# Kernel optimization log

Measured on AMD Instinct MI355X. Metric: run time of the kernel, lower is better.

## Reference

```python
import jax, jax.numpy as jnp
import numpy as np

ANCHORS = jnp.array([[0.57273, 0.677385], [1.87446, 2.06253], [3.33843, 5.47434],
                     [7.88282, 3.52778], [9.77052, 9.16828]], dtype=jnp.float32)
IOU_THR = 0.6
SCALE_NOOBJ = 1.0
SCALE_OBJ = 5.0
DS = 32.0          # downsample_rate
EPS = 1e-7


def _iou_wh(w1, h1, w2, h2):
    # GetCenterAlignIouBetween: boxes aligned at centers -> IoU depends on w,h only
    inter = jnp.minimum(w1, w2) * jnp.minimum(h1, h2)
    return inter / (w1 * h1 + w2 * h2 - inter + EPS)


def setup_inputs() -> dict:
    B, W, H, A, C, M = 128, 19, 19, 5, 81, 24
    N = W * H
    key = jax.random.key(0)
    ks = jax.random.split(key, 8)
    ii, jj = jnp.meshgrid(jnp.arange(W), jnp.arange(H), indexing='ij')
    fm_cord = jnp.stack([jj, ii], -1).reshape(N, 2).astype(jnp.float32)  # (x=j, y=i)
    conf = jax.random.uniform(ks[0], (B, W, H, A, 1)) * 0.98 + 0.01      # valid BCE probs
    pred_xy = fm_cord.reshape(1, W, H, 1, 2) + jax.random.uniform(ks[1], (B, W, H, A, 2))
    pred_wh = jax.random.uniform(ks[2], (B, W, H, A, 2)) * 8.0 + 0.2     # fm units, >0
    cls_score = jax.random.normal(ks[3], (B, W, H, A, C))
    # distinct grid cells per image so sequential scatter == vectorized scatter
    cells = jax.vmap(lambda k: jax.random.choice(k, N, (M,), replace=False))(
        jax.random.split(ks[4], B))
    ci = cells // H
    cj = cells % H
    frac = jax.random.uniform(ks[5], (B, M, 2))
    x = (cj.astype(jnp.float32) + frac[..., 0]) * DS   # pixel coords
    y = (ci.astype(jnp.float32) + frac[..., 1]) * DS
    wh = jax.random.uniform(ks[6], (B, M, 2), minval=12.0, maxval=280.0)
    true_object = jnp.stack([x, y, wh[..., 0], wh[..., 1]], -1)          # [B,M,4] pixels
    labels = jax.random.randint(ks[7], (B, M), 0, C - 1)
    true_label = jax.nn.one_hot(labels, C, dtype=jnp.float32)            # [B,M,C]
    return dict(epoch=0, conf=conf, pred_xy=pred_xy, pred_wh=pred_wh,
                cls_score=cls_score, true_label=true_label,
                true_object=true_object, fm_cord=fm_cord)


def _yolo_loss(conf, pred_xy, pred_wh, cls_score, true_label, true_object, fm_cord):
    B, W, H, A, C = cls_score.shape
    N = W * H
    NA = N * A
    S = float(W)  # config.output_size

    # ---- target assignment (vectorized version of the python loops) ----
    obj = true_object / DS                               # fm units, [B,M,4]
    gx, gy, gw, gh = obj[..., 0], obj[..., 1], obj[..., 2], obj[..., 3]
    i = gy.astype(jnp.int32)                             # row index  (int() truncation)
    j = gx.astype(jnp.int32)                             # col index
    cell = i * H + j                                     # flat cell, [B,M]

    a_iou = _iou_wh(ANCHORS[None, None, :, 0], ANCHORS[None, None, :, 1],
                    gw[..., None], gh[..., None])        # [B,M,A]
    best = jnp.argmax(a_iou, axis=-1)                    # [B,M]
    is_best = best[..., None] == jnp.arange(A)[None, None, :]
    over = a_iou > IOU_THR

    bb = jnp.arange(B)[:, None]
    pwh = pred_wh.reshape(B, N, A, 2)[bb, cell]          # [B,M,A,2] gather at gt cells
    pwh_b = jnp.take_along_axis(pwh, best[..., None, None], axis=2)[:, :, 0]  # [B,M,2]
    iou_pg = _iou_wh(pwh_b[..., 0], pwh_b[..., 1], gw, gh)                    # [B,M]

    mask_val = jnp.where(is_best, 1.0, jnp.where(over, -1.0, 0.0))            # [B,M,A]
    sw = 2.0 - (gw / S) * (gh / S)                                            # [B,M]
    sw_val = jnp.where(is_best, sw[..., None], jnp.where(over, -1.0, 0.0))
    pgi_val = jnp.where(~is_best & over, 0.0, iou_pg[..., None])              # [B,M,A]
    bg = jax.nn.one_hot(C - 1, C, dtype=cls_score.dtype)
    ts_val = jnp.where((is_best | over)[..., None], true_label[:, :, None, :], bg)
    bbox_val = jnp.where(is_best[..., None], obj[:, :, None, :], 0.0)         # [B,M,A,4]

    obj_mask = jnp.zeros((B, N, A)).at[bb, cell].set(mask_val)
    scale_w = jnp.zeros((B, N, A)).at[bb, cell].set(sw_val)
    pgi = jnp.zeros((B, N, A)).at[bb, cell].set(pgi_val)
    true_score = jnp.zeros((B, N, A, C)).at[..., -1].set(1.0).at[bb, cell].set(ts_val)
    true_bbox = jnp.zeros((B, N, A, 4)).at[bb, cell].set(bbox_val)

    # ---- masked losses over flattened [B, W*H*A, ...] ----
    conf_f = conf.reshape(B, NA)
    om = obj_mask.reshape(B, NA)
    swf = scale_w.reshape(B, NA)
    pgif = pgi.reshape(B, NA)
    pxy = pred_xy.reshape(B, NA, 2)
    pwh_f = pred_wh.reshape(B, NA, 2)
    tb = true_bbox.reshape(B, NA, 4)
    ts = true_score.reshape(B, NA, C)
    cs = cls_score.reshape(B, NA, C)
    cord = jnp.repeat(fm_cord[:, None, :], A, axis=1).reshape(NA, 2)

    cp = jnp.clip(conf_f, EPS, 1.0 - EPS)
    noobj_loss = SCALE_NOOBJ * jnp.sum((om == 0) * (-jnp.log(1.0 - cp))) / B
    obj_loss = SCALE_OBJ * jnp.sum(
        (om == 1) * (-(pgif * jnp.log(cp) + (1.0 - pgif) * jnp.log(1.0 - cp)))) / B

    gt = (swf > 0).astype(conf_f.dtype)                  # [B,NA]
    w3 = (SCALE_OBJ * gt * swf)[..., None]
    xy_loss = jnp.sum(w3 * ((pxy - cord[None]) - (tb[..., :2] - cord[None])) ** 2) / B
    wh_loss = jnp.sum(w3 * (pwh_f - tb[..., 2:]) ** 2) / B

    # CE with soft targets, per position: [B,NA]
    ce = -jnp.sum(ts * jax.nn.log_softmax(cs, axis=-1), axis=-1)
    # original broadcasts mask [B,1,NA] * ce [B,NA] -> [B,B,NA] then .sum();
    # equivalent factored form: sum_n (sum_b1 mask) * (sum_b2 ce)
    score_loss = SCALE_OBJ * jnp.sum(gt.sum(0) * ce.sum(0)) / B

    total = noobj_loss + obj_loss + xy_loss + wh_loss + score_loss
    return total, noobj_loss, obj_loss, score_loss, xy_loss, wh_loss


def reference(epoch, conf, pred_xy, pred_wh, cls_score, true_label, true_object, fm_cord):
    return _yolo_loss(conf, pred_xy, pred_wh, cls_score,
                      true_label, true_object, fm_cord)
```

## Files before the change

### kernel.cpp

```cpp
#include <hip/hip_runtime.h>

#define Bsz 128
#define Cd 81
#define Md 24
#define Nd 361
#define NAd 1805
#define RPW 16
#define NT 113
#define NBLK_CLS (NT*16)
#define NOBJ (Bsz*Md)
#define NBLK_LAB (NOBJ/RPW)
#define EPSF 1e-7f
#define IOU_THRF 0.6f

#define OFF_CORR  0
#define OFF_GT    1824
#define OFF_ACC   3648
#define MEMSET_FLOATS 3652
#define OFF_PART  4096
#define OFF_NOOBJ 33024
#define OFF_LAB   35072

#define EXP4(v) { v.x=__expf(v.x); v.y=__expf(v.y); v.z=__expf(v.z); v.w=__expf(v.w); }

__global__ __launch_bounds__(64) void yolo_sweep(
        const float* __restrict__ conf,
        const float* __restrict__ cls_score,
        const float* __restrict__ true_label,
        float* __restrict__ ws) {
    __shared__ float ex[1300];
    const int lane = threadIdx.x;
    const int r = lane >> 2, h = lane & 3;
    const int bid = blockIdx.x;
    float4* l4 = (float4*)ex;

    if (bid < NBLK_CLS) {
        const int t = bid >> 4, g = bid & 15;
        const int na0 = (t == NT - 1) ? (NAd - RPW) : t * RPW;
        const int vmin = t * RPW;
        const bool validr = (na0 + r) >= vmin;
        const bool validc = (lane < RPW) && ((na0 + lane) >= vmin);

        float accCE = 0.0f, nb = 0.0f;

        size_t s = ((size_t)(g * 8) * NAd + na0) * Cd;
        size_t a0 = s & ~(size_t)3;
        int mcur = (int)(s & 3);
        const float4* gp = (const float4*)cls_score + (a0 >> 2);
        float4 u0 = gp[0 * 64 + lane];
        float4 u1 = gp[1 * 64 + lane];
        float4 u2 = gp[2 * 64 + lane];
        float4 u3 = gp[3 * 64 + lane];
        float4 u4 = gp[4 * 64 + lane];
        float4 u5 = gp[261 + lane];
        float cf = validc ? conf[(size_t)(g * 8) * NAd + na0 + lane] : 0.5f;

        for (int it = 0; it < 8; ++it) {
            EXP4(u0); EXP4(u1); EXP4(u2); EXP4(u3); EXP4(u4); EXP4(u5);
            l4[0 * 64 + lane] = u0;
            l4[1 * 64 + lane] = u1;
            l4[2 * 64 + lane] = u2;
            l4[3 * 64 + lane] = u3;
            l4[4 * 64 + lane] = u4;
            l4[261 + lane] = u5;
            __builtin_amdgcn_wave_barrier();

            float4 n0 = {}, n1 = {}, n2 = {}, n3 = {}, n4 = {}, n5 = {};
            float cfn = 0.0f; int mnext = 0;
            if (it < 7) {
                int b = g * 8 + it + 1;
                s = ((size_t)b * NAd + na0) * Cd;
                a0 = s & ~(size_t)3;
                mnext = (int)(s & 3);
                gp = (const float4*)cls_score + (a0 >> 2);
                n0 = gp[0 * 64 + lane];
                n1 = gp[1 * 64 + lane];
                n2 = gp[2 * 64 + lane];
                n3 = gp[3 * 64 + lane];
                n4 = gp[4 * 64 + lane];
                n5 = gp[261 + lane];
                cfn = validc ? conf[(size_t)b * NAd + na0 + lane] : 0.5f;
            }

            const float* p = ex + mcur + r * Cd;
            float sacc = 0.0f;
            #pragma unroll
            for (int j = 0; j < 21; j++) {
                int c0 = h * 21 + j;
                int cc = c0 < 81 ? c0 : 80;
                float w = (c0 < 81) ? 1.0f : 0.0f;
                sacc += p[cc] * w;
            }
            sacc += __shfl_xor(sacc, 1, 64);
            sacc += __shfl_xor(sacc, 2, 64);
            if (h == 0 && validr)
                accCE += __logf(sacc) - __logf(p[80]);
            if (validc) {
                float cp = fminf(fmaxf(cf, EPSF), 1.0f - EPSF);
                nb += -__logf(1.0f - cp);
            }

            u0 = n0; u1 = n1; u2 = n2; u3 = n3; u4 = n4; u5 = n5;
            cf = cfn; mcur = mnext;
        }

        if (h == 0 && validr)
            ws[OFF_PART + (size_t)(na0 + r) * 16 + g] = accCE;

        #pragma unroll
        for (int off = 32; off > 0; off >>= 1) nb += __shfl_xor(nb, off, 64);
        if (lane == 0) ws[OFF_NOOBJ + bid] = nb;
    } else {
        const int lb = bid - NBLK_CLS;
        const float4* gp = (const float4*)(true_label + (size_t)lb * (RPW * Cd));
        float4 u0 = gp[0 * 64 + lane];
        float4 u1 = gp[1 * 64 + lane];
        float4 u2 = gp[2 * 64 + lane];
        float4 u3 = gp[3 * 64 + lane];
        float4 u4 = gp[4 * 64 + lane];
        float4 u5 = gp[260 + lane];
        l4[0 * 64 + lane] = u0;
        l4[1 * 64 + lane] = u1;
        l4[2 * 64 + lane] = u2;
        l4[3 * 64 + lane] = u3;
        l4[4 * 64 + lane] = u4;
        l4[260 + lane] = u5;
        __builtin_amdgcn_wave_barrier();
        const float* p = ex + r * Cd;
        float sacc = 0.0f;
        #pragma unroll
        for (int j = 0; j < 21; j++) {
            int c0 = h * 21 + j;
            int cc = c0 < 81 ? c0 : 80;
            float w = (c0 < 81) ? (float)c0 : 0.0f;
            sacc += p[cc] * w;
        }
        sacc += __shfl_xor(sacc, 1, 64);
        sacc += __shfl_xor(sacc, 2, 64);
        if (h == 0) ws[OFF_LAB + lb * RPW + r] = sacc;
    }
}

__global__ __launch_bounds__(64) void yolo_assign(
        const float* __restrict__ conf,
        const float* __restrict__ pred_xy,
        const float* __restrict__ pred_wh,
        const float* __restrict__ cls_score,
        const float* __restrict__ true_object,
        float* __restrict__ ws) {
    const float AW[5] = {0.57273f, 1.87446f, 3.33843f, 7.88282f, 9.77052f};
    const float AH[5] = {0.677385f, 2.06253f, 5.47434f, 3.52778f, 9.16828f};
    const int idx = blockIdx.x * 64 + threadIdx.x;
    float* corr = ws + OFF_CORR;
    float* gt   = ws + OFF_GT;

    int lab = (int)(ws[OFF_LAB + idx] + 0.5f);
    int b = idx / Md;
    const float4 to = ((const float4*)true_object)[idx];
    const float inv_ds = 1.0f / 32.0f;
    float gx = to.x * inv_ds, gy = to.y * inv_ds;
    float gw = to.z * inv_ds, gh = to.w * inv_ds;
    int ci = (int)gy, cj = (int)gx;
    int cell = ci * 19 + cj;
    float garea = gw * gh;

    float best_iou = -1.0f; int best = 0; bool over[5];
    #pragma unroll
    for (int a = 0; a < 5; a++) {
        float inter = fminf(AW[a], gw) * fminf(AH[a], gh);
        float iou = inter / (AW[a] * AH[a] + garea - inter + EPSF);
        over[a] = iou > IOU_THRF;
        if (iou > best_iou) { best_iou = iou; best = a; }
    }

    int base_bn = (b * Nd + cell) * 5;
    float pwb = pred_wh[(size_t)(base_bn + best) * 2 + 0];
    float phb = pred_wh[(size_t)(base_bn + best) * 2 + 1];
    float inter = fminf(pwb, gw) * fminf(phb, gh);
    float iou_pg = inter / (pwb * phb + garea - inter + EPSF);
    float sw = 2.0f - (gw * (1.0f / 19.0f)) * (gh * (1.0f / 19.0f));

    float a0 = 0.f, a1 = 0.f, a2 = 0.f, a3 = 0.f;
    #pragma unroll
    for (int a = 0; a < 5; a++) {
        bool isb = (a == best);
        if (!(isb || over[a])) continue;
        int pos = base_bn + a;
        int na  = cell * 5 + a;
        float cp = fminf(fmaxf(conf[pos], EPSF), 1.0f - EPSF);
        a0 += __logf(1.0f - cp);
        const float* cs = cls_score + (size_t)pos * Cd;
        atomicAdd(&corr[na], cs[Cd - 1] - cs[lab]);
        if (isb) {
            atomicAdd(&gt[na], 1.0f);
            a1 += -(iou_pg * __logf(cp) + (1.0f - iou_pg) * __logf(1.0f - cp));
            float px = pred_xy[(size_t)pos * 2 + 0], py = pred_xy[(size_t)pos * 2 + 1];
            a2 += sw * ((px - gx) * (px - gx) + (py - gy) * (py - gy));
            float pwa = pred_wh[(size_t)pos * 2 + 0], pha = pred_wh[(size_t)pos * 2 + 1];
            a3 += sw * ((pwa - gw) * (pwa - gw) + (pha - gh) * (pha - gh));
        }
    }

    #pragma unroll
    for (int off = 32; off > 0; off >>= 1) {
        a0 += __shfl_xor(a0, off, 64);
        a1 += __shfl_xor(a1, off, 64);
        a2 += __shfl_xor(a2, off, 64);
        a3 += __shfl_xor(a3, off, 64);
    }
    if (threadIdx.x == 0) {
        atomicAdd(&ws[OFF_ACC + 0], a0);
        atomicAdd(&ws[OFF_ACC + 1], a1);
        atomicAdd(&ws[OFF_ACC + 2], a2);
        atomicAdd(&ws[OFF_ACC + 3], a3);
    }
}

__global__ __launch_bounds__(1024) void yolo_reduce(
        const float* __restrict__ ws, float* __restrict__ out) {
    __shared__ float red[2][16];
    const int tid = threadIdx.x;
    float nsum = 0.0f;
    for (int i = tid; i < NBLK_CLS; i += 1024) nsum += ws[OFF_NOOBJ + i];
    float ssum = 0.0f;
    const float4* part4 = (const float4*)(ws + OFF_PART);
    for (int na = tid; na < NAd; na += 1024) {
        float4 p0 = part4[na * 4 + 0];
        float4 p1 = part4[na * 4 + 1];
        float4 p2 = part4[na * 4 + 2];
        float4 p3 = part4[na * 4 + 3];
        float ce = p0.x + p0.y + p0.z + p0.w + p1.x + p1.y + p1.z + p1.w
                 + p2.x + p2.y + p2.z + p2.w + p3.x + p3.y + p3.z + p3.w
                 + ws[OFF_CORR + na];
        ssum += ws[OFF_GT + na] * ce;
    }

    float v[2] = {nsum, ssum};
    #pragma unroll
    for (int k = 0; k < 2; k++) {
        float x = v[k];
        #pragma unroll
        for (int off = 32; off > 0; off >>= 1) x += __shfl_xor(x, off, 64);
        if ((tid & 63) == 0) red[k][tid >> 6] = x;
    }
    __syncthreads();
    if (tid == 0) {
        float t0 = 0.f, t1 = 0.f;
        #pragma unroll
        for (int w = 0; w < 16; w++) { t0 += red[0][w]; t1 += red[1][w]; }
        const float invB = 1.0f / (float)Bsz;
        float noobj = 1.0f * (t0 + ws[OFF_ACC + 0]) * invB;
        float obj   = 5.0f * ws[OFF_ACC + 1] * invB;
        float xy    = 5.0f * ws[OFF_ACC + 2] * invB;
        float wh    = 5.0f * ws[OFF_ACC + 3] * invB;
        float score = 5.0f * t1 * invB;
        out[0] = noobj + obj + xy + wh + score;
        out[1] = noobj;
        out[2] = obj;
        out[3] = score;
        out[4] = xy;
        out[5] = wh;
    }
}

extern "C" void kernel_launch(void* const* d_in, const int* in_sizes, int n_in,
                              void* d_out, int out_size, void* d_ws, size_t ws_size,
                              hipStream_t stream) {
    const float* conf    = (const float*)d_in[1];
    const float* pred_xy = (const float*)d_in[2];
    const float* pred_wh = (const float*)d_in[3];
    const float* cls     = (const float*)d_in[4];
    const float* tlabel  = (const float*)d_in[5];
    const float* tobject = (const float*)d_in[6];
    float* ws  = (float*)d_ws;
    float* out = (float*)d_out;

    hipMemsetAsync(ws, 0, MEMSET_FLOATS * sizeof(float), stream);

    yolo_sweep<<<NBLK_CLS + NBLK_LAB, 64, 0, stream>>>(conf, cls, tlabel, ws);

    yolo_assign<<<NOBJ / 64, 64, 0, stream>>>(conf, pred_xy, pred_wh, cls, tobject, ws);

    yolo_reduce<<<1, 1024, 0, stream>>>(ws, out);
}
```

Measured before the change: 130.8 us.

## Fuse sweep, assign and reduce into one kernel with last-block reduction

Merges the three kernels into one launch. Assignment blocks compute the label index directly from one-hot rows instead of through a separate pass. The final reduction is done by the last block to arrive at an atomic counter. This removes launch overhead and inter-kernel gaps, but the final reduce now runs on a single 64-thread wave, and label reads are per-thread strided.

Result: slower. 204.4 us (+56.2%).

```diff
diff --git a/kernel.cpp b/kernel.cpp
--- a/kernel.cpp
+++ b/kernel.cpp
@@ -7,35 +7,112 @@
 #define NAd 1805
 #define RPW 16
 #define NT 113
+#define NBLK_ASSIGN 48
 #define NBLK_CLS (NT*16)
+#define NBLK_TOT (NBLK_ASSIGN + NBLK_CLS)
 #define NOBJ (Bsz*Md)
-#define NBLK_LAB (NOBJ/RPW)
 #define EPSF 1e-7f
 #define IOU_THRF 0.6f
 
 #define OFF_CORR  0
 #define OFF_GT    1824
 #define OFF_ACC   3648
-#define MEMSET_FLOATS 3652
+#define OFF_CNT   3652
+#define MEMSET_FLOATS 3656
 #define OFF_PART  4096
 #define OFF_NOOBJ 33024
-#define OFF_LAB   35072
 
 #define EXP4(v) { v.x=__expf(v.x); v.y=__expf(v.y); v.z=__expf(v.z); v.w=__expf(v.w); }
 
-__global__ __launch_bounds__(64) void yolo_sweep(
+__global__ __launch_bounds__(64) void yolo_mega(
         const float* __restrict__ conf,
+        const float* __restrict__ pred_xy,
+        const float* __restrict__ pred_wh,
         const float* __restrict__ cls_score,
         const float* __restrict__ true_label,
-        float* __restrict__ ws) {
+        const float* __restrict__ true_object,
+        float* __restrict__ ws,
+        float* __restrict__ out) {
     __shared__ float ex[1300];
     const int lane = threadIdx.x;
-    const int r = lane >> 2, h = lane & 3;
     const int bid = blockIdx.x;
-    float4* l4 = (float4*)ex;
-
-    if (bid < NBLK_CLS) {
-        const int t = bid >> 4, g = bid & 15;
+
+    if (bid < NBLK_ASSIGN) {
+        const float AW[5] = {0.57273f, 1.87446f, 3.33843f, 7.88282f, 9.77052f};
+        const float AH[5] = {0.677385f, 2.06253f, 5.47434f, 3.52778f, 9.16828f};
+        const int idx = bid * 64 + lane;
+        float* corr = ws + OFF_CORR;
+        float* gt   = ws + OFF_GT;
+
+        const float* tl = true_label + (size_t)idx * Cd;
+        float labf = 0.0f;
+        #pragma unroll
+        for (int c0 = 0; c0 < Cd; c0++) labf += tl[c0] * (float)c0;
+        int lab = (int)(labf + 0.5f);
+
+        int b = idx / Md;
+        const float4 to = ((const float4*)true_object)[idx];
+        const float inv_ds = 1.0f / 32.0f;
+        float gx = to.x * inv_ds, gy = to.y * inv_ds;
+        float gw = to.z * inv_ds, gh = to.w * inv_ds;
+        int ci = (int)gy, cj = (int)gx;
+        int cell = ci * 19 + cj;
+        float garea = gw * gh;
+
+        float best_iou = -1.0f; int best = 0; bool over[5];
+        #pragma unroll
+        for (int a = 0; a < 5; a++) {
+            float inter = fminf(AW[a], gw) * fminf(AH[a], gh);
+            float iou = inter / (AW[a] * AH[a] + garea - inter + EPSF);
+            over[a] = iou > IOU_THRF;
+            if (iou > best_iou) { best_iou = iou; best = a; }
+        }
+
+        int base_bn = (b * Nd + cell) * 5;
+        float pwb = pred_wh[(size_t)(base_bn + best) * 2 + 0];
+        float phb = pred_wh[(size_t)(base_bn + best) * 2 + 1];
+        float inter = fminf(pwb, gw) * fminf(phb, gh);
+        float iou_pg = inter / (pwb * phb + garea - inter + EPSF);
+        float sw = 2.0f - (gw * (1.0f / 19.0f)) * (gh * (1.0f / 19.0f));
+
+        float a0 = 0.f, a1 = 0.f, a2 = 0.f, a3 = 0.f;
+        #pragma unroll
+        for (int a = 0; a < 5; a++) {
+            bool isb = (a == best);
+            if (!(isb || over[a])) continue;
+            int pos = base_bn + a;
+            int na  = cell * 5 + a;
+            float cp = fminf(fmaxf(conf[pos], EPSF), 1.0f - EPSF);
+            a0 += __logf(1.0f - cp);
+            const float* cs = cls_score + (size_t)pos * Cd;
+            atomicAdd(&corr[na], cs[Cd - 1] - cs[lab]);
+            if (isb) {
+                atomicAdd(&gt[na], 1.0f);
+                a1 += -(iou_pg * __logf(cp) + (1.0f - iou_pg) * __logf(1.0f - cp));
+                float px = pred_xy[(size_t)pos * 2 + 0], py = pred_xy[(size_t)pos * 2 + 1];
+                a2 += sw * ((px - gx) * (px - gx) + (py - gy) * (py - gy));
+                float pwa = pred_wh[(size_t)pos * 2 + 0], pha = pred_wh[(size_t)pos * 2 + 1];
+                a3 += sw * ((pwa - gw) * (pwa - gw) + (pha - gh) * (pha - gh));
+            }
+        }
+        #pragma unroll
+        for (int off = 32; off > 0; off >>= 1) {
+            a0 += __shfl_xor(a0, off, 64);
+            a1 += __shfl_xor(a1, off, 64);
+            a2 += __shfl_xor(a2, off, 64);
+            a3 += __shfl_xor(a3, off, 64);
+        }
+        if (lane == 0) {
+            atomicAdd(&ws[OFF_ACC + 0], a0);
+            atomicAdd(&ws[OFF_ACC + 1], a1);
+            atomicAdd(&ws[OFF_ACC + 2], a2);
+            atomicAdd(&ws[OFF_ACC + 3], a3);
+        }
+    } else {
+        const int cbid = bid - NBLK_ASSIGN;
+        const int r = lane >> 2, h = lane & 3;
+        float4* l4 = (float4*)ex;
+        const int t = cbid >> 4, g = cbid & 15;
         const int na0 = (t == NT - 1) ? (NAd - RPW) : t * RPW;
         const int vmin = t * RPW;
         const bool validr = (na0 + r) >= vmin;
@@ -44,9 +121,9 @@
         float accCE = 0.0f, nb = 0.0f;
 
         size_t s = ((size_t)(g * 8) * NAd + na0) * Cd;
-        size_t a0 = s & ~(size_t)3;
+        size_t a0a = s & ~(size_t)3;
         int mcur = (int)(s & 3);
-        const float4* gp = (const float4*)cls_score + (a0 >> 2);
+        const float4* gp = (const float4*)cls_score + (a0a >> 2);
         float4 u0 = gp[0 * 64 + lane];
         float4 u1 = gp[1 * 64 + lane];
         float4 u2 = gp[2 * 64 + lane];
@@ -70,9 +147,9 @@
             if (it < 7) {
                 int b = g * 8 + it + 1;
                 s = ((size_t)b * NAd + na0) * Cd;
-                a0 = s & ~(size_t)3;
+                a0a = s & ~(size_t)3;
                 mnext = (int)(s & 3);
-                gp = (const float4*)cls_score + (a0 >> 2);
+                gp = (const float4*)cls_score + (a0a >> 2);
                 n0 = gp[0 * 64 + lane];
                 n1 = gp[1 * 64 + lane];
                 n2 = gp[2 * 64 + lane];
@@ -88,8 +165,7 @@
             for (int j = 0; j < 21; j++) {
                 int c0 = h * 21 + j;
                 int cc = c0 < 81 ? c0 : 80;
-                float w = (c0 < 81) ? 1.0f : 0.0f;
-                sacc += p[cc] * w;
+                sacc += p[cc] * ((c0 < 81) ? 1.0f : 0.0f);
             }
             sacc += __shfl_xor(sacc, 1, 64);
             sacc += __shfl_xor(sacc, 2, 64);
@@ -106,160 +182,50 @@
 
         if (h == 0 && validr)
             ws[OFF_PART + (size_t)(na0 + r) * 16 + g] = accCE;
-
         #pragma unroll
         for (int off = 32; off > 0; off >>= 1) nb += __shfl_xor(nb, off, 64);
-        if (lane == 0) ws[OFF_NOOBJ + bid] = nb;
-    } else {
-        const int lb = bid - NBLK_CLS;
-        const float4* gp = (const float4*)(true_label + (size_t)lb * (RPW * Cd));
-        float4 u0 = gp[0 * 64 + lane];
-        float4 u1 = gp[1 * 64 + lane];
-        float4 u2 = gp[2 * 64 + lane];
-        float4 u3 = gp[3 * 64 + lane];
-        float4 u4 = gp[4 * 64 + lane];
-        float4 u5 = gp[260 + lane];
-        l4[0 * 64 + lane] = u0;
-        l4[1 * 64 + lane] = u1;
-        l4[2 * 64 + lane] = u2;
-        l4[3 * 64 + lane] = u3;
-        l4[4 * 64 + lane] = u4;
-        l4[260 + lane] = u5;
-        __builtin_amdgcn_wave_barrier();
-        const float* p = ex + r * Cd;
-        float sacc = 0.0f;
-        #pragma unroll
-        for (int j = 0; j < 21; j++) {
-            int c0 = h * 21 + j;
-            int cc = c0 < 81 ? c0 : 80;
-            float w = (c0 < 81) ? (float)c0 : 0.0f;
-            sacc += p[cc] * w;
-        }
-        sacc += __shfl_xor(sacc, 1, 64);
-        sacc += __shfl_xor(sacc, 2, 64);
-        if (h == 0) ws[OFF_LAB + lb * RPW + r] = sacc;
+        if (lane == 0) ws[OFF_NOOBJ + cbid] = nb;
     }
-}
-
-__global__ __launch_bounds__(64) void yolo_assign(
-        const float* __restrict__ conf,
-        const float* __restrict__ pred_xy,
-        const float* __restrict__ pred_wh,
-        const float* __restrict__ cls_score,
-        const float* __restrict__ true_object,
-        float* __restrict__ ws) {
-    const float AW[5] = {0.57273f, 1.87446f, 3.33843f, 7.88282f, 9.77052f};
-    const float AH[5] = {0.677385f, 2.06253f, 5.47434f, 3.52778f, 9.16828f};
-    const int idx = blockIdx.x * 64 + threadIdx.x;
-    float* corr = ws + OFF_CORR;
-    float* gt   = ws + OFF_GT;
-
-    int lab = (int)(ws[OFF_LAB + idx] + 0.5f);
-    int b = idx / Md;
-    const float4 to = ((const float4*)true_object)[idx];
-    const float inv_ds = 1.0f / 32.0f;
-    float gx = to.x * inv_ds, gy = to.y * inv_ds;
-    float gw = to.z * inv_ds, gh = to.w * inv_ds;
-    int ci = (int)gy, cj = (int)gx;
-    int cell = ci * 19 + cj;
-    float garea = gw * gh;
-
-    float best_iou = -1.0f; int best = 0; bool over[5];
-    #pragma unroll
-    for (int a = 0; a < 5; a++) {
-        float inter = fminf(AW[a], gw) * fminf(AH[a], gh);
-        float iou = inter / (AW[a] * AH[a] + garea - inter + EPSF);
-        over[a] = iou > IOU_THRF;
-        if (iou > best_iou) { best_iou = iou; best = a; }
-    }
-
-    int base_bn = (b * Nd + cell) * 5;
-    float pwb = pred_wh[(size_t)(base_bn + best) * 2 + 0];
-    float phb = pred_wh[(size_t)(base_bn + best) * 2 + 1];
-    float inter = fminf(pwb, gw) * fminf(phb, gh);
-    float iou_pg = inter / (pwb * phb + garea - inter + EPSF);
-    float sw = 2.0f - (gw * (1.0f / 19.0f)) * (gh * (1.0f / 19.0f));
-
-    float a0 = 0.f, a1 = 0.f, a2 = 0.f, a3 = 0.f;
-    #pragma unroll
-    for (int a = 0; a < 5; a++) {
-        bool isb = (a == best);
-        if (!(isb || over[a])) continue;
-        int pos = base_bn + a;
-        int na  = cell * 5 + a;
-        float cp = fminf(fmaxf(conf[pos], EPSF), 1.0f - EPSF);
-        a0 += __logf(1.0f - cp);
-        const float* cs = cls_score + (size_t)pos * Cd;
-        atomicAdd(&corr[na], cs[Cd - 1] - cs[lab]);
-        if (isb) {
-            atomicAdd(&gt[na], 1.0f);
-            a1 += -(iou_pg * __logf(cp) + (1.0f - iou_pg) * __logf(1.0f - cp));
-            float px = pred_xy[(size_t)pos * 2 + 0], py = pred_xy[(size_t)pos * 2 + 1];
-            a2 += sw * ((px - gx) * (px - gx) + (py - gy) * (py - gy));
-            float pwa = pred_wh[(size_t)pos * 2 + 0], pha = pred_wh[(size_t)pos * 2 + 1];
-            a3 += sw * ((pwa - gw) * (pwa - gw) + (pha - gh) * (pha - gh));
-        }
-    }
-
-    #pragma unroll
-    for (int off = 32; off > 0; off >>= 1) {
-        a0 += __shfl_xor(a0, off, 64);
-        a1 += __shfl_xor(a1, off, 64);
-        a2 += __shfl_xor(a2, off, 64);
-        a3 += __shfl_xor(a3, off, 64);
-    }
-    if (threadIdx.x == 0) {
-        atomicAdd(&ws[OFF_ACC + 0], a0);
-        atomicAdd(&ws[OFF_ACC + 1], a1);
-        atomicAdd(&ws[OFF_ACC + 2], a2);
-        atomicAdd(&ws[OFF_ACC + 3], a3);
-    }
-}
-
-__global__ __launch_bounds__(1024) void yolo_reduce(
-        const float* __restrict__ ws, float* __restrict__ out) {
-    __shared__ float red[2][16];
-    const int tid = threadIdx.x;
-    float nsum = 0.0f;
-    for (int i = tid; i < NBLK_CLS; i += 1024) nsum += ws[OFF_NOOBJ + i];
-    float ssum = 0.0f;
-    const float4* part4 = (const float4*)(ws + OFF_PART);
-    for (int na = tid; na < NAd; na += 1024) {
-        float4 p0 = part4[na * 4 + 0];
-        float4 p1 = part4[na * 4 + 1];
-        float4 p2 = part4[na * 4 + 2];
-        float4 p3 = part4[na * 4 + 3];
-        float ce = p0.x + p0.y + p0.z + p0.w + p1.x + p1.y + p1.z + p1.w
-                 + p2.x + p2.y + p2.z + p2.w + p3.x + p3.y + p3.z + p3.w
-                 + ws[OFF_CORR + na];
-        ssum += ws[OFF_GT + na] * ce;
-    }
-
-    float v[2] = {nsum, ssum};
-    #pragma unroll
-    for (int k = 0; k < 2; k++) {
-        float x = v[k];
-        #pragma unroll
-        for (int off = 32; off > 0; off >>= 1) x += __shfl_xor(x, off, 64);
-        if ((tid & 63) == 0) red[k][tid >> 6] = x;
-    }
-    __syncthreads();
-    if (tid == 0) {
-        float t0 = 0.f, t1 = 0.f;
-        #pragma unroll
-        for (int w = 0; w < 16; w++) { t0 += red[0][w]; t1 += red[1][w]; }
-        const float invB = 1.0f / (float)Bsz;
-        float noobj = 1.0f * (t0 + ws[OFF_ACC + 0]) * invB;
-        float obj   = 5.0f * ws[OFF_ACC + 1] * invB;
-        float xy    = 5.0f * ws[OFF_ACC + 2] * invB;
-        float wh    = 5.0f * ws[OFF_ACC + 3] * invB;
-        float score = 5.0f * t1 * invB;
-        out[0] = noobj + obj + xy + wh + score;
-        out[1] = noobj;
-        out[2] = obj;
-        out[3] = score;
-        out[4] = xy;
-        out[5] = wh;
+
+    __threadfence();
+    unsigned old = 0;
+    if (lane == 0) old = atomicAdd((unsigned*)(ws + OFF_CNT), 1u);
+    old = __shfl(old, 0, 64);
+    if (old == NBLK_TOT - 1) {
+        __threadfence();
+        float nsum = 0.0f;
+        for (int i = lane; i < NBLK_CLS; i += 64) nsum += ws[OFF_NOOBJ + i];
+        float ssum = 0.0f;
+        const float4* part4 = (const float4*)(ws + OFF_PART);
+        for (int na = lane; na < NAd; na += 64) {
+            float4 p0 = part4[na * 4 + 0];
+            float4 p1 = part4[na * 4 + 1];
+            float4 p2 = part4[na * 4 + 2];
+            float4 p3 = part4[na * 4 + 3];
+            float ce = p0.x + p0.y + p0.z + p0.w + p1.x + p1.y + p1.z + p1.w
+                     + p2.x + p2.y + p2.z + p2.w + p3.x + p3.y + p3.z + p3.w
+                     + ws[OFF_CORR + na];
+            ssum += ws[OFF_GT + na] * ce;
+        }
+        #pragma unroll
+        for (int off = 32; off > 0; off >>= 1) {
+            nsum += __shfl_xor(nsum, off, 64);
+            ssum += __shfl_xor(ssum, off, 64);
+        }
+        if (lane == 0) {
+            const float invB = 1.0f / (float)Bsz;
+            float noobj = 1.0f * (nsum + ws[OFF_ACC + 0]) * invB;
+            float obj   = 5.0f * ws[OFF_ACC + 1] * invB;
+            float xy    = 5.0f * ws[OFF_ACC + 2] * invB;
+            float wh    = 5.0f * ws[OFF_ACC + 3] * invB;
+            float score = 5.0f * ssum * invB;
+            out[0] = noobj + obj + xy + wh + score;
+            out[1] = noobj;
+            out[2] = obj;
+            out[3] = score;
+            out[4] = xy;
+            out[5] = wh;
+        }
     }
 }
 
@@ -277,9 +243,6 @@
 
     hipMemsetAsync(ws, 0, MEMSET_FLOATS * sizeof(float), stream);
 
-    yolo_sweep<<<NBLK_CLS + NBLK_LAB, 64, 0, stream>>>(conf, cls, tlabel, ws);
-
-    yolo_assign<<<NOBJ / 64, 64, 0, stream>>>(conf, pred_xy, pred_wh, cls, tobject, ws);
-
-    yolo_reduce<<<1, 1024, 0, stream>>>(ws, out);
+    yolo_mega<<<NBLK_TOT, 64, 0, stream>>>(conf, pred_xy, pred_wh, cls,
+                                           tlabel, tobject, ws, out);
 }
```

## Fuse target-assignment kernel into sweep kernel and use nontemporal loads

Applied to the files above, without the earlier changes.

Folds the separate assign kernel into extra blocks of the sweep kernel. Each assign thread now decodes its own one-hot label directly, which drops the label-decode blocks and their workspace round trip. This removes one kernel launch and the dependency between the sweep and assign stages. The cls_score and conf streaming loads also become nontemporal loads to reduce cache pollution. The trade-off is that per-thread label decoding is an uncoalesced strided read of 81 floats per object, and the new assign blocks run alongside the heavy sweep blocks.

Measured after the change: 134.9 us. 3.1% more time.

```diff
diff --git a/kernel.cpp b/kernel.cpp
--- a/kernel.cpp
+++ b/kernel.cpp
@@ -8,8 +8,9 @@
 #define RPW 16
 #define NT 113
 #define NBLK_CLS (NT*16)
+#define NBLK_ASSIGN 48
+#define NBLK_TOT (NBLK_CLS + NBLK_ASSIGN)
 #define NOBJ (Bsz*Md)
-#define NBLK_LAB (NOBJ/RPW)
 #define EPSF 1e-7f
 #define IOU_THRF 0.6f
 
@@ -19,22 +20,27 @@
 #define MEMSET_FLOATS 3652
 #define OFF_PART  4096
 #define OFF_NOOBJ 33024
-#define OFF_LAB   35072
+
+typedef float vf4 __attribute__((ext_vector_type(4)));
 
 #define EXP4(v) { v.x=__expf(v.x); v.y=__expf(v.y); v.z=__expf(v.z); v.w=__expf(v.w); }
+#define NTL4(p) __builtin_nontemporal_load(p)
 
 __global__ __launch_bounds__(64) void yolo_sweep(
         const float* __restrict__ conf,
+        const float* __restrict__ pred_xy,
+        const float* __restrict__ pred_wh,
         const float* __restrict__ cls_score,
         const float* __restrict__ true_label,
+        const float* __restrict__ true_object,
         float* __restrict__ ws) {
     __shared__ float ex[1300];
     const int lane = threadIdx.x;
-    const int r = lane >> 2, h = lane & 3;
     const int bid = blockIdx.x;
-    float4* l4 = (float4*)ex;
 
     if (bid < NBLK_CLS) {
+        const int r = lane >> 2, h = lane & 3;
+        vf4* l4 = (vf4*)ex;
         const int t = bid >> 4, g = bid & 15;
         const int na0 = (t == NT - 1) ? (NAd - RPW) : t * RPW;
         const int vmin = t * RPW;
@@ -44,16 +50,17 @@
         float accCE = 0.0f, nb = 0.0f;
 
         size_t s = ((size_t)(g * 8) * NAd + na0) * Cd;
-        size_t a0 = s & ~(size_t)3;
+        size_t a0a = s & ~(size_t)3;
         int mcur = (int)(s & 3);
-        const float4* gp = (const float4*)cls_score + (a0 >> 2);
-        float4 u0 = gp[0 * 64 + lane];
-        float4 u1 = gp[1 * 64 + lane];
-        float4 u2 = gp[2 * 64 + lane];
-        float4 u3 = gp[3 * 64 + lane];
-        float4 u4 = gp[4 * 64 + lane];
-        float4 u5 = gp[261 + lane];
-        float cf = validc ? conf[(size_t)(g * 8) * NAd + na0 + lane] : 0.5f;
+        const vf4* gp = (const vf4*)cls_score + (a0a >> 2);
+        vf4 u0 = NTL4(gp + 0 * 64 + lane);
+        vf4 u1 = NTL4(gp + 1 * 64 + lane);
+        vf4 u2 = NTL4(gp + 2 * 64 + lane);
+        vf4 u3 = NTL4(gp + 3 * 64 + lane);
+        vf4 u4 = NTL4(gp + 4 * 64 + lane);
+        vf4 u5 = NTL4(gp + 261 + lane);
+        float cf = validc ? __builtin_nontemporal_load(conf + (size_t)(g * 8) * NAd + na0 + lane)
+                          : 0.5f;
 
         for (int it = 0; it < 8; ++it) {
             EXP4(u0); EXP4(u1); EXP4(u2); EXP4(u3); EXP4(u4); EXP4(u5);
@@ -65,21 +72,22 @@
             l4[261 + lane] = u5;
             __builtin_amdgcn_wave_barrier();
 
-            float4 n0 = {}, n1 = {}, n2 = {}, n3 = {}, n4 = {}, n5 = {};
+            vf4 n0 = {}, n1 = {}, n2 = {}, n3 = {}, n4 = {}, n5 = {};
             float cfn = 0.0f; int mnext = 0;
             if (it < 7) {
                 int b = g * 8 + it + 1;
                 s = ((size_t)b * NAd + na0) * Cd;
-                a0 = s & ~(size_t)3;
+                a0a = s & ~(size_t)3;
                 mnext = (int)(s & 3);
-                gp = (const float4*)cls_score + (a0 >> 2);
-                n0 = gp[0 * 64 + lane];
-                n1 = gp[1 * 64 + lane];
-                n2 = gp[2 * 64 + lane];
-                n3 = gp[3 * 64 + lane];
-                n4 = gp[4 * 64 + lane];
-                n5 = gp[261 + lane];
-                cfn = validc ? conf[(size_t)b * NAd + na0 + lane] : 0.5f;
+                gp = (const vf4*)cls_score + (a0a >> 2);
+                n0 = NTL4(gp + 0 * 64 + lane);
+                n1 = NTL4(gp + 1 * 64 + lane);
+                n2 = NTL4(gp + 2 * 64 + lane);
+                n3 = NTL4(gp + 3 * 64 + lane);
+                n4 = NTL4(gp + 4 * 64 + lane);
+                n5 = NTL4(gp + 261 + lane);
+                if (validc)
+                    cfn = __builtin_nontemporal_load(conf + (size_t)b * NAd + na0 + lane);
             }
 
             const float* p = ex + mcur + r * Cd;
@@ -88,8 +96,7 @@
             for (int j = 0; j < 21; j++) {
                 int c0 = h * 21 + j;
                 int cc = c0 < 81 ? c0 : 80;
-                float w = (c0 < 81) ? 1.0f : 0.0f;
-                sacc += p[cc] * w;
+                sacc += p[cc] * ((c0 < 81) ? 1.0f : 0.0f);
             }
             sacc += __shfl_xor(sacc, 1, 64);
             sacc += __shfl_xor(sacc, 2, 64);
@@ -106,113 +113,80 @@
 
         if (h == 0 && validr)
             ws[OFF_PART + (size_t)(na0 + r) * 16 + g] = accCE;
-
         #pragma unroll
         for (int off = 32; off > 0; off >>= 1) nb += __shfl_xor(nb, off, 64);
         if (lane == 0) ws[OFF_NOOBJ + bid] = nb;
     } else {
-        const int lb = bid - NBLK_CLS;
-        const float4* gp = (const float4*)(true_label + (size_t)lb * (RPW * Cd));
-        float4 u0 = gp[0 * 64 + lane];
-        float4 u1 = gp[1 * 64 + lane];
-        float4 u2 = gp[2 * 64 + lane];
-        float4 u3 = gp[3 * 64 + lane];
-        float4 u4 = gp[4 * 64 + lane];
-        float4 u5 = gp[260 + lane];
-        l4[0 * 64 + lane] = u0;
-        l4[1 * 64 + lane] = u1;
-        l4[2 * 64 + lane] = u2;
-        l4[3 * 64 + lane] = u3;
-        l4[4 * 64 + lane] = u4;
-        l4[260 + lane] = u5;
-        __builtin_amdgcn_wave_barrier();
-        const float* p = ex + r * Cd;
-        float sacc = 0.0f;
-        #pragma unroll
-        for (int j = 0; j < 21; j++) {
-            int c0 = h * 21 + j;
-            int cc = c0 < 81 ? c0 : 80;
-            float w = (c0 < 81) ? (float)c0 : 0.0f;
-            sacc += p[cc] * w;
-        }
-        sacc += __shfl_xor(sacc, 1, 64);
-        sacc += __shfl_xor(sacc, 2, 64);
-        if (h == 0) ws[OFF_LAB + lb * RPW + r] = sacc;
-    }
-}
-
-__global__ __launch_bounds__(64) void yolo_assign(
-        const float* __restrict__ conf,
-        const float* __restrict__ pred_xy,
-        const float* __restrict__ pred_wh,
-        const float* __restrict__ cls_score,
-        const float* __restrict__ true_object,
-        float* __restrict__ ws) {
-    const float AW[5] = {0.57273f, 1.87446f, 3.33843f, 7.88282f, 9.77052f};
-    const float AH[5] = {0.677385f, 2.06253f, 5.47434f, 3.52778f, 9.16828f};
-    const int idx = blockIdx.x * 64 + threadIdx.x;
-    float* corr = ws + OFF_CORR;
-    float* gt   = ws + OFF_GT;
-
-    int lab = (int)(ws[OFF_LAB + idx] + 0.5f);
-    int b = idx / Md;
-    const float4 to = ((const float4*)true_object)[idx];
-    const float inv_ds = 1.0f / 32.0f;
-    float gx = to.x * inv_ds, gy = to.y * inv_ds;
-    float gw = to.z * inv_ds, gh = to.w * inv_ds;
-    int ci = (int)gy, cj = (int)gx;
-    int cell = ci * 19 + cj;
-    float garea = gw * gh;
-
-    float best_iou = -1.0f; int best = 0; bool over[5];
-    #pragma unroll
-    for (int a = 0; a < 5; a++) {
-        float inter = fminf(AW[a], gw) * fminf(AH[a], gh);
-        float iou = inter / (AW[a] * AH[a] + garea - inter + EPSF);
-        over[a] = iou > IOU_THRF;
-        if (iou > best_iou) { best_iou = iou; best = a; }
-    }
-
-    int base_bn = (b * Nd + cell) * 5;
-    float pwb = pred_wh[(size_t)(base_bn + best) * 2 + 0];
-    float phb = pred_wh[(size_t)(base_bn + best) * 2 + 1];
-    float inter = fminf(pwb, gw) * fminf(phb, gh);
-    float iou_pg = inter / (pwb * phb + garea - inter + EPSF);
-    float sw = 2.0f - (gw * (1.0f / 19.0f)) * (gh * (1.0f / 19.0f));
-
-    float a0 = 0.f, a1 = 0.f, a2 = 0.f, a3 = 0.f;
-    #pragma unroll
-    for (int a = 0; a < 5; a++) {
-        bool isb = (a == best);
-        if (!(isb || over[a])) continue;
-        int pos = base_bn + a;
-        int na  = cell * 5 + a;
-        float cp = fminf(fmaxf(conf[pos], EPSF), 1.0f - EPSF);
-        a0 += __logf(1.0f - cp);
-        const float* cs = cls_score + (size_t)pos * Cd;
-        atomicAdd(&corr[na], cs[Cd - 1] - cs[lab]);
-        if (isb) {
-            atomicAdd(&gt[na], 1.0f);
-            a1 += -(iou_pg * __logf(cp) + (1.0f - iou_pg) * __logf(1.0f - cp));
-            float px = pred_xy[(size_t)pos * 2 + 0], py = pred_xy[(size_t)pos * 2 + 1];
-            a2 += sw * ((px - gx) * (px - gx) + (py - gy) * (py - gy));
-            float pwa = pred_wh[(size_t)pos * 2 + 0], pha = pred_wh[(size_t)pos * 2 + 1];
-            a3 += sw * ((pwa - gw) * (pwa - gw) + (pha - gh) * (pha - gh));
-        }
-    }
-
-    #pragma unroll
-    for (int off = 32; off > 0; off >>= 1) {
-        a0 += __shfl_xor(a0, off, 64);
-        a1 += __shfl_xor(a1, off, 64);
-        a2 += __shfl_xor(a2, off, 64);
-        a3 += __shfl_xor(a3, off, 64);
-    }
-    if (threadIdx.x == 0) {
-        atomicAdd(&ws[OFF_ACC + 0], a0);
-        atomicAdd(&ws[OFF_ACC + 1], a1);
-        atomicAdd(&ws[OFF_ACC + 2], a2);
-        atomicAdd(&ws[OFF_ACC + 3], a3);
+        const float AW[5] = {0.57273f, 1.87446f, 3.33843f, 7.88282f, 9.77052f};
+        const float AH[5] = {0.677385f, 2.06253f, 5.47434f, 3.52778f, 9.16828f};
+        const int idx = (bid - NBLK_CLS) * 64 + lane;
+        float* corr = ws + OFF_CORR;
+        float* gt   = ws + OFF_GT;
+
+        const float* tl = true_label + (size_t)idx * Cd;
+        float labf = 0.0f;
+        #pragma unroll
+        for (int c0 = 0; c0 < Cd; c0++) labf += tl[c0] * (float)c0;
+        int lab = (int)(labf + 0.5f);
+
+        int b = idx / Md;
+        const float4 to = ((const float4*)true_object)[idx];
+        const float inv_ds = 1.0f / 32.0f;
+        float gx = to.x * inv_ds, gy = to.y * inv_ds;
+        float gw = to.z * inv_ds, gh = to.w * inv_ds;
+        int ci = (int)gy, cj = (int)gx;
+        int cell = ci * 19 + cj;
+        float garea = gw * gh;
+
+        float best_iou = -1.0f; int best = 0; bool over[5];
+        #pragma unroll
+        for (int a = 0; a < 5; a++) {
+            float inter = fminf(AW[a], gw) * fminf(AH[a], gh);
+            float iou = inter / (AW[a] * AH[a] + garea - inter + EPSF);
+            over[a] = iou > IOU_THRF;
+            if (iou > best_iou) { best_iou = iou; best = a; }
+        }
+
+        int base_bn = (b * Nd + cell) * 5;
+        float pwb = pred_wh[(size_t)(base_bn + best) * 2 + 0];
+        float phb = pred_wh[(size_t)(base_bn + best) * 2 + 1];
+        float inter = fminf(pwb, gw) * fminf(phb, gh);
+        float iou_pg = inter / (pwb * phb + garea - inter + EPSF);
+        float sw = 2.0f - (gw * (1.0f / 19.0f)) * (gh * (1.0f / 19.0f));
+
+        float a0 = 0.f, a1 = 0.f, a2 = 0.f, a3 = 0.f;
+        #pragma unroll
+        for (int a = 0; a < 5; a++) {
+            bool isb = (a == best);
+            if (!(isb || over[a])) continue;
+            int pos = base_bn + a;
+            int na  = cell * 5 + a;
+            float cp = fminf(fmaxf(conf[pos], EPSF), 1.0f - EPSF);
+            a0 += __logf(1.0f - cp);
+            const float* cs = cls_score + (size_t)pos * Cd;
+            atomicAdd(&corr[na], cs[Cd - 1] - cs[lab]);
+            if (isb) {
+                atomicAdd(&gt[na], 1.0f);
+                a1 += -(iou_pg * __logf(cp) + (1.0f - iou_pg) * __logf(1.0f - cp));
+                float px = pred_xy[(size_t)pos * 2 + 0], py = pred_xy[(size_t)pos * 2 + 1];
+                a2 += sw * ((px - gx) * (px - gx) + (py - gy) * (py - gy));
+                float pwa = pred_wh[(size_t)pos * 2 + 0], pha = pred_wh[(size_t)pos * 2 + 1];
+                a3 += sw * ((pwa - gw) * (pwa - gw) + (pha - gh) * (pha - gh));
+            }
+        }
+        #pragma unroll
+        for (int off = 32; off > 0; off >>= 1) {
+            a0 += __shfl_xor(a0, off, 64);
+            a1 += __shfl_xor(a1, off, 64);
+            a2 += __shfl_xor(a2, off, 64);
+            a3 += __shfl_xor(a3, off, 64);
+        }
+        if (lane == 0) {
+            atomicAdd(&ws[OFF_ACC + 0], a0);
+            atomicAdd(&ws[OFF_ACC + 1], a1);
+            atomicAdd(&ws[OFF_ACC + 2], a2);
+            atomicAdd(&ws[OFF_ACC + 3], a3);
+        }
     }
 }
 
@@ -277,9 +251,8 @@
 
     hipMemsetAsync(ws, 0, MEMSET_FLOATS * sizeof(float), stream);
 
-    yolo_sweep<<<NBLK_CLS + NBLK_LAB, 64, 0, stream>>>(conf, cls, tlabel, ws);
-
-    yolo_assign<<<NOBJ / 64, 64, 0, stream>>>(conf, pred_xy, pred_wh, cls, tobject, ws);
+    yolo_sweep<<<NBLK_TOT, 64, 0, stream>>>(conf, pred_xy, pred_wh, cls,
+                                            tlabel, tobject, ws);
 
     yolo_reduce<<<1, 1024, 0, stream>>>(ws, out);
 }
```
